# Kernel optimization log

Measured on AMD Instinct MI355X. Metric: run time of the kernel, lower is better.

## Reference

```python
import jax, jax.numpy as jnp
import numpy as np

B, D, KM1 = 8192, 256, 64  # batch, feature dim (no bias), num_classes-1
NC = KM1 + 1


def setup_inputs() -> dict:
    key = jax.random.key(0)
    k1, k2, k3 = jax.random.split(key, 3)
    features = jax.random.normal(k1, (B, D), dtype=jnp.float32)
    y = jax.random.randint(k2, (B,), 0, NC)
    mu = jax.random.normal(k3, (D, KM1), dtype=jnp.float32) * 0.001
    Sigma = jnp.broadcast_to(jnp.eye(D, dtype=jnp.float32), (KM1, D, D)).copy()
    return {"features": features, "y": y, "mu": mu, "Sigma": Sigma, "loss_type": 1}


def _b_ky(nc):
    # (nc, nc-1) stick-breaking selector matrix
    return 1.0 - jnp.pad(jnp.eye(nc)[..., :-2], [(0, 0), (1, 0)]).cumsum(-1)


def reference(features, y, mu, Sigma, loss_type):
    x = features                      # use_bias=False -> pad is a no-op
    logits = x @ mu                   # (B, K-1)
    bky = _b_ky(NC)                   # (K, K-1)
    y1h = jax.nn.one_hot(y, NC)       # (B, K)
    if loss_type == 0:
        full = jnp.pad(logits, [(0, 0), (0, 1)]) - jax.nn.softplus(logits) @ bky.T
        return -jnp.sum(full * y1h, -1)
    else:
        # psi_k = sqrt(x^T (Sigma_k + mu_k mu_k^T) x) = sqrt(x^T Sigma_k x + (x.mu_k)^2)
        xSx = jnp.einsum('bd,kde,be->bk', x, Sigma, x)   # (B, K-1)
        psi = jnp.sqrt(xSx + logits * logits)
        b = y1h @ bky                 # (B, K-1)
        kappa = y1h[..., :-1] - b / 2
        return -jnp.sum(logits * kappa + b * (psi / 2 - jax.nn.softplus(psi)), -1)
```

## Files before the change

### kernel.cpp

```cpp
#include <hip/hip_runtime.h>

typedef __attribute__((ext_vector_type(8))) short bf16x8;
typedef __attribute__((ext_vector_type(4))) float f32x4;

#define B_N 8192
#define D_N 256
#define K_N 64

__device__ __forceinline__ unsigned short bf16_rne(float f) {
  unsigned u = __builtin_bit_cast(unsigned, f);
  u += 0x7fffu + ((u >> 16) & 1u);
  return (unsigned short)(u >> 16);
}
__device__ __forceinline__ float bf16_f32(unsigned short h) {
  return __builtin_bit_cast(float, (unsigned)h << 16);
}

__device__ __forceinline__ void gload_lds16(const void* g, void* l) {
  __builtin_amdgcn_global_load_lds(
      (const __attribute__((address_space(1))) unsigned int*)g,
      (__attribute__((address_space(3))) unsigned int*)l, 16, 0, 0);
}

__global__ void convert_kernel(const float* __restrict__ src,
                               ushort* __restrict__ hi, ushort* __restrict__ lo,
                               int n4) {
  int idx = blockIdx.x * blockDim.x + threadIdx.x;
  int stride = gridDim.x * blockDim.x;
  for (int i = idx; i < n4; i += stride) {
    float4 v = ((const float4*)src)[i];
    ushort4 h, l;
    h.x = bf16_rne(v.x); l.x = bf16_rne(v.x - bf16_f32(h.x));
    h.y = bf16_rne(v.y); l.y = bf16_rne(v.y - bf16_f32(h.y));
    h.z = bf16_rne(v.z); l.z = bf16_rne(v.z - bf16_f32(h.z));
    h.w = bf16_rne(v.w); l.w = bf16_rne(v.w - bf16_f32(h.w));
    ((ushort4*)hi)[i] = h;
    ((ushort4*)lo)[i] = l;
  }
}

__global__ void convert_T_kernel(const float* __restrict__ Sigma,
                                 ushort* __restrict__ Th,
                                 ushort* __restrict__ Tl) {
  const int dtab[10] = {0, 0, 0, 0, 1, 1, 1, 2, 2, 3};
  const int etab[10] = {0, 1, 2, 3, 1, 2, 3, 2, 3, 3};
  const int k = blockIdx.x;
  const int dblk = dtab[blockIdx.y], eblk = etab[blockIdx.y];
  const float wgt = (dblk == eblk) ? 0.5f : 1.0f;
  const int tid = threadIdx.x;
  const int dl = tid >> 2;
  const int el0 = (tid & 3) * 16;
  const int d = dblk * 64 + dl;
  const size_t rowbase = ((size_t)k * D_N + d) * D_N + eblk * 64 + el0;
  const float* Srow = Sigma + rowbase;
  const float* Scol = Sigma + ((size_t)k * D_N + eblk * 64 + el0) * D_N + d;
  ushort h[16], l[16];
#pragma unroll
  for (int i = 0; i < 16; ++i) {
    const float t = (Srow[i] + Scol[(size_t)i * D_N]) * wgt;
    h[i] = bf16_rne(t);
    l[i] = bf16_rne(t - bf16_f32(h[i]));
  }
  *(uint4*)(Th + rowbase) = *(uint4*)&h[0];
  *(uint4*)(Th + rowbase + 8) = *(uint4*)&h[8];
  *(uint4*)(Tl + rowbase) = *(uint4*)&l[0];
  *(uint4*)(Tl + rowbase + 8) = *(uint4*)&l[8];
}

__global__ __launch_bounds__(256, 3) void xsx_tri_kernel(
    const float* __restrict__ X,
    const ushort* __restrict__ Xh, const ushort* __restrict__ Xl,
    const ushort* __restrict__ Th, const ushort* __restrict__ Tl,
    float* __restrict__ part) {
  __shared__ __align__(16) ushort smem[20480];
  ushort(*A_h)[32] = (ushort(*)[32])(smem);
  ushort(*A_l)[32] = (ushort(*)[32])(smem + 8192);
  ushort(*B_h)[32] = (ushort(*)[32])(smem + 16384);
  ushort(*B_l)[32] = (ushort(*)[32])(smem + 18432);

  const int tid = threadIdx.x;
  const int lane = tid & 63;
  const int wid = tid >> 6;
  const int lr = lane & 15;
  const int lk = lane >> 4;

  const int bid = blockIdx.x;
  const int xcd = bid & 7;
  const int r = bid >> 3;
  const int qd = r >> 8;
  const int s = r & 255;
  const int kk = xcd * 8 + (s & 7);
  const int bg = s >> 3;
  const int bbase = bg * 256;

  const int srow = lane >> 2;
  const int sc = ((lane & 3) ^ ((lane >> 3) & 3)) * 8;
  const int rdc = (lk ^ ((lr >> 1) & 3)) * 8;

  f32x4 acc[4][4];
#pragma unroll
  for (int mi = 0; mi < 4; ++mi)
#pragma unroll
    for (int ni = 0; ni < 4; ++ni) acc[mi][ni] = (f32x4){0.f, 0.f, 0.f, 0.f};

  const size_t a0 = (size_t)(bbase + wid * 64 + srow) * D_N + sc;
  const size_t b0g = (size_t)kk * (D_N * D_N) +
                     (size_t)(qd * 64 + wid * 16 + srow) * D_N + sc;

  const int nch = 2 * (4 - qd);
  for (int c = 0; c < nch; ++c) {
    const int e0 = qd * 64 + c * 32;
    __syncthreads();
#pragma unroll
    for (int i = 0; i < 4; ++i) {
      gload_lds16(Xh + a0 + i * 16 * D_N + e0, &A_h[wid * 64 + i * 16][0]);
      gload_lds16(Xl + a0 + i * 16 * D_N + e0, &A_l[wid * 64 + i * 16][0]);
    }
    gload_lds16(Th + b0g + e0, &B_h[wid * 16][0]);
    gload_lds16(Tl + b0g + e0, &B_l[wid * 16][0]);
    __syncthreads();

    bf16x8 ah[4], al[4];
#pragma unroll
    for (int mi = 0; mi < 4; ++mi) {
      ah[mi] = *(const bf16x8*)&A_h[wid * 64 + mi * 16 + lr][rdc];
      al[mi] = *(const bf16x8*)&A_l[wid * 64 + mi * 16 + lr][rdc];
    }
#pragma unroll
    for (int ni = 0; ni < 4; ++ni) {
      const bf16x8 bh = *(const bf16x8*)&B_h[ni * 16 + lr][rdc];
      const bf16x8 bl = *(const bf16x8*)&B_l[ni * 16 + lr][rdc];
#pragma unroll
      for (int mi = 0; mi < 4; ++mi)
        acc[mi][ni] = __builtin_amdgcn_mfma_f32_16x16x32_bf16(
            ah[mi], bh, acc[mi][ni], 0, 0, 0);
#pragma unroll
      for (int mi = 0; mi < 4; ++mi)
        acc[mi][ni] = __builtin_amdgcn_mfma_f32_16x16x32_bf16(
            al[mi], bh, acc[mi][ni], 0, 0, 0);
#pragma unroll
      for (int mi = 0; mi < 4; ++mi)
        acc[mi][ni] = __builtin_amdgcn_mfma_f32_16x16x32_bf16(
            ah[mi], bl, acc[mi][ni], 0, 0, 0);
    }
  }

#pragma unroll
  for (int mi = 0; mi < 4; ++mi) {
#pragma unroll
    for (int jj = 0; jj < 4; ++jj) {
      const int brow = bbase + wid * 64 + mi * 16 + lk * 4 + jj;
      const float* xr = X + (size_t)brow * D_N + qd * 64 + lr;
      float p = 0.f;
#pragma unroll
      for (int ni = 0; ni < 4; ++ni) p = fmaf(acc[mi][ni][jj], xr[ni * 16], p);
      p += __shfl_xor(p, 1);
      p += __shfl_xor(p, 2);
      p += __shfl_xor(p, 4);
      p += __shfl_xor(p, 8);
      if (lr == 0) part[((size_t)brow * K_N + kk) * 4 + qd] = p;
    }
  }
}

__global__ __launch_bounds__(512, 2) void xsx_fallback(
    const float* __restrict__ X, const float* __restrict__ Sigma,
    float* __restrict__ xsx) {
  constexpr int BM = 128, KT = 32;
  __shared__ __align__(16) ushort Ah[BM][KT];
  __shared__ __align__(16) ushort Al[BM][KT];
  __shared__ __align__(16) ushort Bh[D_N][KT];
  __shared__ __align__(16) ushort Bl[D_N][KT];
  __shared__ float red[4][BM];

  const int tid = threadIdx.x;
  const int lane = tid & 63;
  const int wid = tid >> 6;
  const int wm = wid >> 2;
  const int wn = wid & 3;
  const int lr = lane & 15;
  const int lk = lane >> 4;

  const int b0 = blockIdx.x * BM;
  const int kk = blockIdx.y;
  const size_t soff = (size_t)kk * D_N * D_N;

  f32x4 acc[4][4];
#pragma unroll
  for (int mi = 0; mi < 4; ++mi)
#pragma unroll
    for (int ni = 0; ni < 4; ++ni) acc[mi][ni] = (f32x4){0.f, 0.f, 0.f, 0.f};

  for (int ec = 0; ec < D_N / KT; ++ec) {
    const int e0 = ec * KT;
    __syncthreads();
#pragma unroll
    for (int r = 0; r < 2; ++r) {
      const int i = tid + 512 * r;
      const int row = i >> 3, c4 = (i & 7) * 4;
      const float4 v = *(const float4*)(X + (size_t)(b0 + row) * D_N + e0 + c4);
      ushort4 h, l;
      h.x = bf16_rne(v.x); l.x = bf16_rne(v.x - bf16_f32(h.x));
      h.y = bf16_rne(v.y); l.y = bf16_rne(v.y - bf16_f32(h.y));
      h.z = bf16_rne(v.z); l.z = bf16_rne(v.z - bf16_f32(h.z));
      h.w = bf16_rne(v.w); l.w = bf16_rne(v.w - bf16_f32(h.w));
      *(ushort4*)&Ah[row][c4] = h;
      *(ushort4*)&Al[row][c4] = l;
    }
#pragma unroll
    for (int r = 0; r < 4; ++r) {
      const int i = tid + 512 * r;
      const int d = i >> 3, c4 = (i & 7) * 4;
      const float4 v = *(const float4*)(Sigma + soff + (size_t)d * D_N + e0 + c4);
      ushort4 h, l;
      h.x = bf16_rne(v.x); l.x = bf16_rne(v.x - bf16_f32(h.x));
      h.y = bf16_rne(v.y); l.y = bf16_rne(v.y - bf16_f32(h.y));
      h.z = bf16_rne(v.z); l.z = bf16_rne(v.z - bf16_f32(h.z));
      h.w = bf16_rne(v.w); l.w = bf16_rne(v.w - bf16_f32(h.w));
      *(ushort4*)&Bh[d][c4] = h;
      *(ushort4*)&Bl[d][c4] = l;
    }
    __syncthreads();

    bf16x8 ah[4], al[4];
#pragma unroll
    for (int mi = 0; mi < 4; ++mi) {
      ah[mi] = *(const bf16x8*)&Ah[wm * 64 + mi * 16 + lr][lk * 8];
      al[mi] = *(const bf16x8*)&Al[wm * 64 + mi * 16 + lr][lk * 8];
    }
#pragma unroll
    for (int ni = 0; ni < 4; ++ni) {
      const bf16x8 bh = *(const bf16x8*)&Bh[wn * 64 + ni * 16 + lr][lk * 8];
      const bf16x8 bl = *(const bf16x8*)&Bl[wn * 64 + ni * 16 + lr][lk * 8];
#pragma unroll
      for (int mi = 0; mi < 4; ++mi) {
        acc[mi][ni] = __builtin_amdgcn_mfma_f32_16x16x32_bf16(ah[mi], bh, acc[mi][ni], 0, 0, 0);
        acc[mi][ni] = __builtin_amdgcn_mfma_f32_16x16x32_bf16(al[mi], bh, acc[mi][ni], 0, 0, 0);
        acc[mi][ni] = __builtin_amdgcn_mfma_f32_16x16x32_bf16(ah[mi], bl, acc[mi][ni], 0, 0, 0);
      }
    }
  }

  float p[4][4];
#pragma unroll
  for (int mi = 0; mi < 4; ++mi)
#pragma unroll
    for (int jj = 0; jj < 4; ++jj) p[mi][jj] = 0.f;
#pragma unroll
  for (int mi = 0; mi < 4; ++mi) {
#pragma unroll
    for (int jj = 0; jj < 4; ++jj) {
      const int brow = b0 + wm * 64 + mi * 16 + lk * 4 + jj;
      const float* xr = X + (size_t)brow * D_N + wn * 64 + lr;
#pragma unroll
      for (int ni = 0; ni < 4; ++ni)
        p[mi][jj] = fmaf(acc[mi][ni][jj], xr[ni * 16], p[mi][jj]);
    }
  }
#pragma unroll
  for (int mi = 0; mi < 4; ++mi)
#pragma unroll
    for (int jj = 0; jj < 4; ++jj) {
      float v = p[mi][jj];
      v += __shfl_xor(v, 1);
      v += __shfl_xor(v, 2);
      v += __shfl_xor(v, 4);
      v += __shfl_xor(v, 8);
      p[mi][jj] = v;
    }
  if (lr == 0) {
#pragma unroll
    for (int mi = 0; mi < 4; ++mi)
#pragma unroll
      for (int jj = 0; jj < 4; ++jj)
        red[wn][wm * 64 + mi * 16 + lk * 4 + jj] = p[mi][jj];
  }
  __syncthreads();
  if (tid < BM) {
    const float s = red[0][tid] + red[1][tid] + red[2][tid] + red[3][tid];
    xsx[(size_t)(b0 + tid) * K_N + kk] = s;
  }
}

__global__ __launch_bounds__(256) void loss_kernel(
    const float* __restrict__ X, const int* __restrict__ y,
    const float* __restrict__ mu, const int* __restrict__ loss_type,
    const float* __restrict__ xsx, float* __restrict__ out, int nparts) {
  __shared__ float mu_s[D_N * K_N];
  __shared__ float x_s[4][D_N];
  const int tid = threadIdx.x;
  const int wid = tid >> 6;
  const int lane = tid & 63;
  const int b = blockIdx.x * 4 + wid;

  for (int i = tid; i < D_N * K_N / 4; i += 256)
    ((float4*)mu_s)[i] = ((const float4*)mu)[i];
  ((float4*)&x_s[wid][0])[lane] = ((const float4*)(X + (size_t)b * D_N))[lane];
  __syncthreads();

  const int yb = y[b];
  const int lt = loss_type[0];

  float logit = 0.f;
#pragma unroll 8
  for (int d = 0; d < D_N; ++d)
    logit = fmaf(x_s[wid][d], mu_s[d * K_N + lane], logit);

  float term;
  if (lt == 1) {
    float xv;
    if (nparts == 4) {
      const float4 pv = *(const float4*)(xsx + ((size_t)b * K_N + lane) * 4);
      xv = ((pv.x + pv.y) + pv.z) + pv.w;
    } else {
      xv = xsx[(size_t)b * K_N + lane];
    }
    const float psi = sqrtf(fmaxf(xv + logit * logit, 0.f));
    const float bk = (lane <= yb) ? 1.f : 0.f;
    const float kap = ((lane == yb) ? 1.f : 0.f) - 0.5f * bk;
    term = logit * kap + bk * (-0.5f * psi - log1pf(expf(-psi)));
  } else {
    const float sp = (logit > 0.f) ? (logit + log1pf(expf(-logit)))
                                   : log1pf(expf(logit));
    term = ((lane == yb) ? logit : 0.f) - ((lane <= yb) ? sp : 0.f);
  }
#pragma unroll
  for (int s = 1; s < 64; s <<= 1) term += __shfl_xor(term, s);
  if (lane == 0) out[b] = -term;
}

extern "C" void kernel_launch(void* const* d_in, const int* in_sizes, int n_in,
                              void* d_out, int out_size, void* d_ws, size_t ws_size,
                              hipStream_t stream) {
  const float* X = (const float*)d_in[0];
  const int* y = (const int*)d_in[1];
  const float* mu = (const float*)d_in[2];
  const float* Sigma = (const float*)d_in[3];
  const int* lt = (const int*)d_in[4];
  float* out = (float*)d_out;

  const size_t XN = (size_t)B_N * D_N;
  const size_t SN = (size_t)K_N * D_N * D_N;
  const size_t xh_off = 0;
  const size_t xl_off = xh_off + XN * 2;
  const size_t th_off = xl_off + XN * 2;
  const size_t tl_off = th_off + SN * 2;
  const size_t part_off = tl_off + SN * 2;
  const size_t need = part_off + (size_t)B_N * K_N * 4 * 4;

  char* w = (char*)d_ws;
  if (ws_size >= need) {
    ushort* Xh = (ushort*)(w + xh_off);
    ushort* Xl = (ushort*)(w + xl_off);
    ushort* Th = (ushort*)(w + th_off);
    ushort* Tl = (ushort*)(w + tl_off);
    float* part = (float*)(w + part_off);
    hipLaunchKernelGGL(convert_kernel, dim3(1024), dim3(256), 0, stream,
                       X, Xh, Xl, (int)(XN / 4));
    hipLaunchKernelGGL(convert_T_kernel, dim3(64, 10), dim3(256), 0, stream,
                       Sigma, Th, Tl);
    hipLaunchKernelGGL(xsx_tri_kernel, dim3(8192), dim3(256), 0, stream,
                       X, Xh, Xl, Th, Tl, part);
    hipLaunchKernelGGL(loss_kernel, dim3(B_N / 4), dim3(256), 0, stream,
                       X, y, mu, lt, part, out, 4);
  } else {
    float* xsx = (float*)w;
    hipLaunchKernelGGL(xsx_fallback, dim3(B_N / 128, K_N), dim3(512), 0, stream,
                       X, Sigma, xsx);
    hipLaunchKernelGGL(loss_kernel, dim3(B_N / 4), dim3(256), 0, stream,
                       X, y, mu, lt, xsx, out, 1);
  }
}
```

Measured before the change: 194.0 us.

## Load X fragments directly from global and double-buffer Sigma tiles in LDS

Each wave's A tile (the X hi/lo bf16 fragments) was private to that wave. It is now read straight from global memory into registers instead of being staged through LDS. The B tile (Th/Tl) is double-buffered in LDS, so the next chunk is prefetched while the current one is being computed, and each iteration needs one barrier instead of two. This cuts LDS traffic and the size of the shared allocation, which could raise occupancy. The cost is global-load latency now sitting directly in front of the MFMAs, with no prefetch for the X fragments.

Result: slower. 247.3 us (+27.5%).

```diff
diff --git a/kernel.cpp b/kernel.cpp
--- a/kernel.cpp
+++ b/kernel.cpp
@@ -72,11 +72,7 @@
     const ushort* __restrict__ Xh, const ushort* __restrict__ Xl,
     const ushort* __restrict__ Th, const ushort* __restrict__ Tl,
     float* __restrict__ part) {
-  __shared__ __align__(16) ushort smem[20480];
-  ushort(*A_h)[32] = (ushort(*)[32])(smem);
-  ushort(*A_l)[32] = (ushort(*)[32])(smem + 8192);
-  ushort(*B_h)[32] = (ushort(*)[32])(smem + 16384);
-  ushort(*B_l)[32] = (ushort(*)[32])(smem + 18432);
+  __shared__ __align__(16) ushort Bbuf[2][2][64 * 32];
 
   const int tid = threadIdx.x;
   const int lane = tid & 63;
@@ -103,33 +99,40 @@
 #pragma unroll
     for (int ni = 0; ni < 4; ++ni) acc[mi][ni] = (f32x4){0.f, 0.f, 0.f, 0.f};
 
-  const size_t a0 = (size_t)(bbase + wid * 64 + srow) * D_N + sc;
   const size_t b0g = (size_t)kk * (D_N * D_N) +
                      (size_t)(qd * 64 + wid * 16 + srow) * D_N + sc;
+  const size_t a0 = (size_t)(bbase + wid * 64 + lr) * D_N + lk * 8;
 
   const int nch = 2 * (4 - qd);
+
+  {
+    const int e0 = qd * 64;
+    gload_lds16(Th + b0g + e0, &Bbuf[0][0][wid * 16 * 32]);
+    gload_lds16(Tl + b0g + e0, &Bbuf[0][1][wid * 16 * 32]);
+  }
+  __syncthreads();
+
   for (int c = 0; c < nch; ++c) {
+    const int cur = c & 1;
+    if (c + 1 < nch) {
+      const int e1 = qd * 64 + (c + 1) * 32;
+      gload_lds16(Th + b0g + e1, &Bbuf[cur ^ 1][0][wid * 16 * 32]);
+      gload_lds16(Tl + b0g + e1, &Bbuf[cur ^ 1][1][wid * 16 * 32]);
+    }
     const int e0 = qd * 64 + c * 32;
-    __syncthreads();
-#pragma unroll
-    for (int i = 0; i < 4; ++i) {
-      gload_lds16(Xh + a0 + i * 16 * D_N + e0, &A_h[wid * 64 + i * 16][0]);
-      gload_lds16(Xl + a0 + i * 16 * D_N + e0, &A_l[wid * 64 + i * 16][0]);
-    }
-    gload_lds16(Th + b0g + e0, &B_h[wid * 16][0]);
-    gload_lds16(Tl + b0g + e0, &B_l[wid * 16][0]);
-    __syncthreads();
 
     bf16x8 ah[4], al[4];
 #pragma unroll
-    for (int mi = 0; mi < 4; ++mi) {
-      ah[mi] = *(const bf16x8*)&A_h[wid * 64 + mi * 16 + lr][rdc];
-      al[mi] = *(const bf16x8*)&A_l[wid * 64 + mi * 16 + lr][rdc];
-    }
+    for (int mi = 0; mi < 4; ++mi)
+      ah[mi] = *(const bf16x8*)(Xh + a0 + (size_t)(mi * 16) * D_N + e0);
+#pragma unroll
+    for (int mi = 0; mi < 4; ++mi)
+      al[mi] = *(const bf16x8*)(Xl + a0 + (size_t)(mi * 16) * D_N + e0);
+
 #pragma unroll
     for (int ni = 0; ni < 4; ++ni) {
-      const bf16x8 bh = *(const bf16x8*)&B_h[ni * 16 + lr][rdc];
-      const bf16x8 bl = *(const bf16x8*)&B_l[ni * 16 + lr][rdc];
+      const bf16x8 bh = *(const bf16x8*)&Bbuf[cur][0][(ni * 16 + lr) * 32 + rdc];
+      const bf16x8 bl = *(const bf16x8*)&Bbuf[cur][1][(ni * 16 + lr) * 32 + rdc];
 #pragma unroll
       for (int mi = 0; mi < 4; ++mi)
         acc[mi][ni] = __builtin_amdgcn_mfma_f32_16x16x32_bf16(
@@ -143,6 +146,7 @@
         acc[mi][ni] = __builtin_amdgcn_mfma_f32_16x16x32_bf16(
             ah[mi], bl, acc[mi][ni], 0, 0, 0);
     }
+    __syncthreads();
   }
 
 #pragma unroll
```

## Retile xSx kernel to process two classes per block with smaller batch tile

Applied to the files above, without the earlier changes.

Each block now computes 128 batch rows for two Sigma slices instead of 256 rows for one, so the X tile in LDS is reused across two classes. LDS per block shrinks and launch bounds allow four blocks per CU for higher occupancy. Sigma tiles are now fetched twice as often per batch row, which shifts load traffic toward the Sigma side.

Result: slower. 202.1 us (+4.2%).

```diff
diff --git a/kernel.cpp b/kernel.cpp
--- a/kernel.cpp
+++ b/kernel.cpp
@@ -67,16 +67,15 @@
   *(uint4*)(Tl + rowbase + 8) = *(uint4*)&l[8];
 }
 
-__global__ __launch_bounds__(256, 3) void xsx_tri_kernel(
+__global__ __launch_bounds__(256, 4) void xsx_tri2_kernel(
     const float* __restrict__ X,
     const ushort* __restrict__ Xh, const ushort* __restrict__ Xl,
     const ushort* __restrict__ Th, const ushort* __restrict__ Tl,
     float* __restrict__ part) {
-  __shared__ __align__(16) ushort smem[20480];
-  ushort(*A_h)[32] = (ushort(*)[32])(smem);
-  ushort(*A_l)[32] = (ushort(*)[32])(smem + 8192);
-  ushort(*B_h)[32] = (ushort(*)[32])(smem + 16384);
-  ushort(*B_l)[32] = (ushort(*)[32])(smem + 18432);
+  __shared__ __align__(16) ushort A_h[128][32];
+  __shared__ __align__(16) ushort A_l[128][32];
+  __shared__ __align__(16) ushort B_h[2][64][32];
+  __shared__ __align__(16) ushort B_l[2][64][32];
 
   const int tid = threadIdx.x;
   const int lane = tid & 63;
@@ -88,77 +87,89 @@
   const int xcd = bid & 7;
   const int r = bid >> 3;
   const int qd = r >> 8;
-  const int s = r & 255;
-  const int kk = xcd * 8 + (s & 7);
-  const int bg = s >> 3;
-  const int bbase = bg * 256;
+  const int kp = (r >> 6) & 3;
+  const int bg = r & 63;
+  const int kk0 = xcd * 8 + kp * 2;
+  const int bbase = bg * 128;
 
   const int srow = lane >> 2;
   const int sc = ((lane & 3) ^ ((lane >> 3) & 3)) * 8;
   const int rdc = (lk ^ ((lr >> 1) & 3)) * 8;
 
-  f32x4 acc[4][4];
-#pragma unroll
-  for (int mi = 0; mi < 4; ++mi)
-#pragma unroll
-    for (int ni = 0; ni < 4; ++ni) acc[mi][ni] = (f32x4){0.f, 0.f, 0.f, 0.f};
-
-  const size_t a0 = (size_t)(bbase + wid * 64 + srow) * D_N + sc;
-  const size_t b0g = (size_t)kk * (D_N * D_N) +
+  f32x4 acc[2][2][4];
+#pragma unroll
+  for (int kp2 = 0; kp2 < 2; ++kp2)
+#pragma unroll
+    for (int mi = 0; mi < 2; ++mi)
+#pragma unroll
+      for (int ni = 0; ni < 4; ++ni)
+        acc[kp2][mi][ni] = (f32x4){0.f, 0.f, 0.f, 0.f};
+
+  const size_t a0 = (size_t)(bbase + wid * 32 + srow) * D_N + sc;
+  const size_t bK0 = (size_t)kk0 * (D_N * D_N) +
                      (size_t)(qd * 64 + wid * 16 + srow) * D_N + sc;
+  const size_t bK1 = bK0 + (size_t)(D_N * D_N);
 
   const int nch = 2 * (4 - qd);
   for (int c = 0; c < nch; ++c) {
     const int e0 = qd * 64 + c * 32;
     __syncthreads();
-#pragma unroll
-    for (int i = 0; i < 4; ++i) {
-      gload_lds16(Xh + a0 + i * 16 * D_N + e0, &A_h[wid * 64 + i * 16][0]);
-      gload_lds16(Xl + a0 + i * 16 * D_N + e0, &A_l[wid * 64 + i * 16][0]);
-    }
-    gload_lds16(Th + b0g + e0, &B_h[wid * 16][0]);
-    gload_lds16(Tl + b0g + e0, &B_l[wid * 16][0]);
+    gload_lds16(Xh + a0 + e0, &A_h[wid * 32][0]);
+    gload_lds16(Xh + a0 + (size_t)16 * D_N + e0, &A_h[wid * 32 + 16][0]);
+    gload_lds16(Xl + a0 + e0, &A_l[wid * 32][0]);
+    gload_lds16(Xl + a0 + (size_t)16 * D_N + e0, &A_l[wid * 32 + 16][0]);
+    gload_lds16(Th + bK0 + e0, &B_h[0][wid * 16][0]);
+    gload_lds16(Tl + bK0 + e0, &B_l[0][wid * 16][0]);
+    gload_lds16(Th + bK1 + e0, &B_h[1][wid * 16][0]);
+    gload_lds16(Tl + bK1 + e0, &B_l[1][wid * 16][0]);
     __syncthreads();
 
-    bf16x8 ah[4], al[4];
-#pragma unroll
-    for (int mi = 0; mi < 4; ++mi) {
-      ah[mi] = *(const bf16x8*)&A_h[wid * 64 + mi * 16 + lr][rdc];
-      al[mi] = *(const bf16x8*)&A_l[wid * 64 + mi * 16 + lr][rdc];
-    }
-#pragma unroll
-    for (int ni = 0; ni < 4; ++ni) {
-      const bf16x8 bh = *(const bf16x8*)&B_h[ni * 16 + lr][rdc];
-      const bf16x8 bl = *(const bf16x8*)&B_l[ni * 16 + lr][rdc];
-#pragma unroll
-      for (int mi = 0; mi < 4; ++mi)
-        acc[mi][ni] = __builtin_amdgcn_mfma_f32_16x16x32_bf16(
-            ah[mi], bh, acc[mi][ni], 0, 0, 0);
-#pragma unroll
-      for (int mi = 0; mi < 4; ++mi)
-        acc[mi][ni] = __builtin_amdgcn_mfma_f32_16x16x32_bf16(
-            al[mi], bh, acc[mi][ni], 0, 0, 0);
-#pragma unroll
-      for (int mi = 0; mi < 4; ++mi)
-        acc[mi][ni] = __builtin_amdgcn_mfma_f32_16x16x32_bf16(
-            ah[mi], bl, acc[mi][ni], 0, 0, 0);
-    }
-  }
-
-#pragma unroll
-  for (int mi = 0; mi < 4; ++mi) {
-#pragma unroll
-    for (int jj = 0; jj < 4; ++jj) {
-      const int brow = bbase + wid * 64 + mi * 16 + lk * 4 + jj;
-      const float* xr = X + (size_t)brow * D_N + qd * 64 + lr;
-      float p = 0.f;
-#pragma unroll
-      for (int ni = 0; ni < 4; ++ni) p = fmaf(acc[mi][ni][jj], xr[ni * 16], p);
-      p += __shfl_xor(p, 1);
-      p += __shfl_xor(p, 2);
-      p += __shfl_xor(p, 4);
-      p += __shfl_xor(p, 8);
-      if (lr == 0) part[((size_t)brow * K_N + kk) * 4 + qd] = p;
+    bf16x8 ah[2], al[2];
+#pragma unroll
+    for (int mi = 0; mi < 2; ++mi) {
+      ah[mi] = *(const bf16x8*)&A_h[wid * 32 + mi * 16 + lr][rdc];
+      al[mi] = *(const bf16x8*)&A_l[wid * 32 + mi * 16 + lr][rdc];
+    }
+#pragma unroll
+    for (int kp2 = 0; kp2 < 2; ++kp2) {
+#pragma unroll
+      for (int ni = 0; ni < 4; ++ni) {
+        const bf16x8 bh = *(const bf16x8*)&B_h[kp2][ni * 16 + lr][rdc];
+        const bf16x8 bl = *(const bf16x8*)&B_l[kp2][ni * 16 + lr][rdc];
+#pragma unroll
+        for (int mi = 0; mi < 2; ++mi)
+          acc[kp2][mi][ni] = __builtin_amdgcn_mfma_f32_16x16x32_bf16(
+              ah[mi], bh, acc[kp2][mi][ni], 0, 0, 0);
+#pragma unroll
+        for (int mi = 0; mi < 2; ++mi)
+          acc[kp2][mi][ni] = __builtin_amdgcn_mfma_f32_16x16x32_bf16(
+              al[mi], bh, acc[kp2][mi][ni], 0, 0, 0);
+#pragma unroll
+        for (int mi = 0; mi < 2; ++mi)
+          acc[kp2][mi][ni] = __builtin_amdgcn_mfma_f32_16x16x32_bf16(
+              ah[mi], bl, acc[kp2][mi][ni], 0, 0, 0);
+      }
+    }
+  }
+
+#pragma unroll
+  for (int kp2 = 0; kp2 < 2; ++kp2) {
+#pragma unroll
+    for (int mi = 0; mi < 2; ++mi) {
+#pragma unroll
+      for (int jj = 0; jj < 4; ++jj) {
+        const int brow = bbase + wid * 32 + mi * 16 + lk * 4 + jj;
+        const float* xr = X + (size_t)brow * D_N + qd * 64 + lr;
+        float p = 0.f;
+#pragma unroll
+        for (int ni = 0; ni < 4; ++ni)
+          p = fmaf(acc[kp2][mi][ni][jj], xr[ni * 16], p);
+        p += __shfl_xor(p, 1);
+        p += __shfl_xor(p, 2);
+        p += __shfl_xor(p, 4);
+        p += __shfl_xor(p, 8);
+        if (lr == 0) part[((size_t)brow * K_N + kk0 + kp2) * 4 + qd] = p;
+      }
     }
   }
 }
@@ -359,7 +370,7 @@
                        X, Xh, Xl, (int)(XN / 4));
     hipLaunchKernelGGL(convert_T_kernel, dim3(64, 10), dim3(256), 0, stream,
                        Sigma, Th, Tl);
-    hipLaunchKernelGGL(xsx_tri_kernel, dim3(8192), dim3(256), 0, stream,
+    hipLaunchKernelGGL(xsx_tri2_kernel, dim3(8192), dim3(256), 0, stream,
                        X, Xh, Xl, Th, Tl, part);
     hipLaunchKernelGGL(loss_kernel, dim3(B_N / 4), dim3(256), 0, stream,
                        X, y, mu, lt, part, out, 4);
```
